# Kernel optimization log

Measured on AMD Instinct MI355X. Metric: run time of the kernel, lower is better.

Reference implementation:

```python
import jax, jax.numpy as jnp
import numpy as np

BITS = 8
BOUND = 2 ** (BITS - 1) - 1  # 127, symmetric int8 as in AQT IntNumerics


def setup_inputs() -> dict:
    key = jax.random.key(0)
    k1, k2 = jax.random.split(key)
    lhs = jax.random.normal(k1, (8192, 4096), dtype=jnp.float32)
    rhs = jax.random.normal(k2, (4096, 4096), dtype=jnp.float32)
    return {"lhs": lhs, "rhs": rhs}


def reference(lhs, rhs):
    # Per-channel symmetric scales over the contracting dim (AQT calibration:
    # abs-max / bound). lhs contracts axis 1, rhs contracts axis 0, per
    # dimension_numbers (((1,),(0,)),((),())).
    lhs_scale = jnp.max(jnp.abs(lhs), axis=1, keepdims=True) / BOUND  # [M,1]
    rhs_scale = jnp.max(jnp.abs(rhs), axis=0, keepdims=True) / BOUND  # [1,N]
    lhs_scale = jnp.where(lhs_scale == 0, jnp.ones_like(lhs_scale), lhs_scale)
    rhs_scale = jnp.where(rhs_scale == 0, jnp.ones_like(rhs_scale), rhs_scale)

    # Quantize: round-to-nearest, clip to [-127, 127], store as int8.
    qlhs = jnp.clip(jnp.round(lhs / lhs_scale), -BOUND, BOUND).astype(jnp.int8)
    qrhs = jnp.clip(jnp.round(rhs / rhs_scale), -BOUND, BOUND).astype(jnp.int8)

    # Integer matmul with int32 accumulation (the AQT quantized dot_general).
    acc = jax.lax.dot_general(
        qlhs, qrhs,
        dimension_numbers=(((1,), (0,)), ((), ())),
        preferred_element_type=jnp.int32,
    )  # [M, N] int32

    # Inline dequant by transposed scales (scale_t): [M,1] * [1,N].
    return acc.astype(jnp.float32) * lhs_scale * rhs_scale
```

## Files before the change

### kernel.cpp

```cpp
#include <hip/hip_runtime.h>
#include <stdint.h>

#define M_DIM 8192
#define N_DIM 4096
#define K_DIM 4096

typedef int v4i __attribute__((ext_vector_type(4)));

typedef __attribute__((address_space(1))) const void gas_void;
typedef __attribute__((address_space(3))) void las_void;

__device__ __forceinline__ void async_copy16(const uint8_t* g, uint8_t* l) {
    __builtin_amdgcn_global_load_lds((gas_void*)g, (las_void*)l, 16, 0, 0);
}

__device__ __forceinline__ int quant1(float x, float scale) {
    float q = __builtin_rintf(x / scale);
    q = fminf(127.0f, fmaxf(-127.0f, q));
    return (int)q;
}

__device__ __forceinline__ uint32_t pack4(int q0, int q1, int q2, int q3) {
    return (uint32_t)(q0 & 255) | ((uint32_t)(q1 & 255) << 8) |
           ((uint32_t)(q2 & 255) << 16) | ((uint32_t)(q3 & 255) << 24);
}

__global__ __launch_bounds__(256) void quant_lhs_kernel(
    const float* __restrict__ lhs, uint8_t* __restrict__ qlhs,
    float* __restrict__ lhs_scale) {
    const int row = blockIdx.x;
    const int tid = threadIdx.x;
    const float4* src = (const float4*)(lhs + (size_t)row * K_DIM);

    float4 v[4];
    float m = 0.0f;
#pragma unroll
    for (int i = 0; i < 4; ++i) {
        v[i] = src[tid + i * 256];
        m = fmaxf(m, fmaxf(fmaxf(fabsf(v[i].x), fabsf(v[i].y)),
                           fmaxf(fabsf(v[i].z), fabsf(v[i].w))));
    }
#pragma unroll
    for (int off = 32; off > 0; off >>= 1)
        m = fmaxf(m, __shfl_down(m, off, 64));

    __shared__ float wmax[4];
    if ((tid & 63) == 0) wmax[tid >> 6] = m;
    __syncthreads();
    const float mm = fmaxf(fmaxf(wmax[0], wmax[1]), fmaxf(wmax[2], wmax[3]));
    const float scale = (mm == 0.0f) ? 1.0f : mm / 127.0f;
    if (tid == 0) lhs_scale[row] = scale;

    uint32_t* dst = (uint32_t*)(qlhs + (size_t)row * K_DIM);
#pragma unroll
    for (int i = 0; i < 4; ++i) {
        dst[tid + i * 256] = pack4(quant1(v[i].x, scale), quant1(v[i].y, scale),
                                   quant1(v[i].z, scale), quant1(v[i].w, scale));
    }
}

__global__ __launch_bounds__(256) void rhs_max_kernel(
    const float* __restrict__ rhs, uint32_t* __restrict__ maxbits) {
    const int c4 = (blockIdx.x * 256 + threadIdx.x) * 4;
    const int r0 = blockIdx.y * 32;
    float m0 = 0.0f, m1 = 0.0f, m2 = 0.0f, m3 = 0.0f;
#pragma unroll
    for (int r = 0; r < 32; ++r) {
        const float4 v = *(const float4*)(rhs + (size_t)(r0 + r) * N_DIM + c4);
        m0 = fmaxf(m0, fabsf(v.x));
        m1 = fmaxf(m1, fabsf(v.y));
        m2 = fmaxf(m2, fabsf(v.z));
        m3 = fmaxf(m3, fabsf(v.w));
    }
    atomicMax(&maxbits[c4 + 0], __float_as_uint(m0));
    atomicMax(&maxbits[c4 + 1], __float_as_uint(m1));
    atomicMax(&maxbits[c4 + 2], __float_as_uint(m2));
    atomicMax(&maxbits[c4 + 3], __float_as_uint(m3));
}

__global__ __launch_bounds__(256) void quant_rhs_t_kernel(
    const float* __restrict__ rhs, const uint32_t* __restrict__ maxbits,
    uint8_t* __restrict__ qrhsT) {
    __shared__ __align__(16) uint8_t tile[64 * 132];
    const int nbase = blockIdx.x * 64;
    const int kbase = blockIdx.y * 128;
    const int tid = threadIdx.x;

    const int n0 = (tid & 15) * 4;
    float s[4];
#pragma unroll
    for (int j = 0; j < 4; ++j) {
        const float m = __uint_as_float(maxbits[nbase + n0 + j]);
        s[j] = (m == 0.0f) ? 1.0f : m / 127.0f;
    }

#pragma unroll
    for (int p = 0; p < 2; ++p) {
        const int k0 = (tid >> 4) * 4 + p * 64;
        int q[4][4];
#pragma unroll
        for (int i = 0; i < 4; ++i) {
            const float4 v = *(const float4*)(
                rhs + (size_t)(kbase + k0 + i) * N_DIM + nbase + n0);
            q[i][0] = quant1(v.x, s[0]);
            q[i][1] = quant1(v.y, s[1]);
            q[i][2] = quant1(v.z, s[2]);
            q[i][3] = quant1(v.w, s[3]);
        }
#pragma unroll
        for (int j = 0; j < 4; ++j) {
            *(uint32_t*)(tile + (n0 + j) * 132 + k0) =
                pack4(q[0][j], q[1][j], q[2][j], q[3][j]);
        }
    }
    __syncthreads();

#pragma unroll
    for (int p = 0; p < 2; ++p) {
        const int c = tid + p * 256;
        const int n = c >> 3;
        const int g = c & 7;
        uint32_t d[4];
#pragma unroll
        for (int w = 0; w < 4; ++w)
            d[w] = *(const uint32_t*)(tile + n * 132 + g * 16 + w * 4);
        uint4 u;
        u.x = d[0]; u.y = d[1]; u.z = d[2]; u.w = d[3];
        *(uint4*)(qrhsT + (size_t)(nbase + n) * K_DIM + kbase + g * 16) = u;
    }
}

__global__ __launch_bounds__(512, 2) void gemm_i8_kernel(
    const uint8_t* __restrict__ qlhs, const uint8_t* __restrict__ qrhsT,
    const float* __restrict__ lhs_scale, const uint32_t* __restrict__ maxbits,
    float* __restrict__ out) {
    extern __shared__ __align__(16) uint8_t smem[];

    const int tid = threadIdx.x;
    const int wave = tid >> 6;
    const int lane = tid & 63;

    const int obid = blockIdx.y * 16 + blockIdx.x;
    const int xcd = obid & 7;
    const int local = obid >> 3;
    const int ty = (xcd >> 1) * 8 + (local >> 3);
    const int tx = (xcd & 1) * 8 + (local & 7);
    const int bm = ty * 256;
    const int bn = tx * 256;

    const int srow = tid >> 2;
    const int gsrc = (((tid & 3) ^ ((tid >> 3) & 3)) << 4);
    const uint8_t* gA = qlhs + (size_t)(bm + srow) * K_DIM + gsrc;
    const uint8_t* gA2 = gA + (size_t)128 * K_DIM;
    const uint8_t* gB = qrhsT + (size_t)(bn + srow) * K_DIM + gsrc;
    const uint8_t* gB2 = gB + (size_t)128 * K_DIM;
    const uint32_t stO = (uint32_t)tid * 16u;

    const int wm = (wave >> 2) * 128;
    const int wn = (wave & 3) * 64;
    const uint32_t fg = (uint32_t)((((lane >> 4) ^ ((lane >> 1) & 3)) << 4));
    const uint32_t aoff = (uint32_t)((wm + (lane & 15)) * 64) + fg;
    const uint32_t boff = 16384u + (uint32_t)((wn + (lane & 15)) * 64) + fg;

    v4i acc[8][4] = {};

    v4i Xb0, Xb1, Xb2, Xb3, Xa0, Xa1;
    v4i Yb0, Yb1, Yb2, Yb3, Ya0, Ya1;

#define FENCE() asm volatile("" ::: "memory")
#define LGKM(n)                                                 \
    do {                                                        \
        asm volatile("s_waitcnt lgkmcnt(" #n ")" ::: "memory"); \
        __builtin_amdgcn_sched_barrier(0);                      \
    } while (0)
#define MFMA4(C, mi, av)                                                       \
    do {                                                                       \
        acc[mi][0] = __builtin_amdgcn_mfma_i32_16x16x64_i8(av, C##b0,          \
                                                           acc[mi][0], 0, 0, 0); \
        acc[mi][1] = __builtin_amdgcn_mfma_i32_16x16x64_i8(av, C##b1,          \
                                                           acc[mi][1], 0, 0, 0); \
        acc[mi][2] = __builtin_amdgcn_mfma_i32_16x16x64_i8(av, C##b2,          \
                                                           acc[mi][2], 0, 0, 0); \
        acc[mi][3] = __builtin_amdgcn_mfma_i32_16x16x64_i8(av, C##b3,          \
                                                           acc[mi][3], 0, 0, 0); \
    } while (0)

#define TILE(u, C, N)                                                   \
    do {                                                                \
        const uint8_t* const Cb = smem + ((u) << 15);                   \
        const uint8_t* const Nb = smem + ((((u) + 1) & 3) << 15);       \
        uint8_t* const Sb = smem + ((((u) + 3) & 3) << 15);             \
               \
        async_copy16(gA, Sb + stO);                                     \
        async_copy16(gA2, Sb + 8192 + stO);                             \
        async_copy16(gB, Sb + 16384 + stO);                             \
        async_copy16(gB2, Sb + 24576 + stO);                            \
        if (tt + (u) < 60) {                                            \
            gA += 64; gA2 += 64; gB += 64; gB2 += 64;                   \
        }                                                               \
        FENCE();                                                        \
        v4i va2, va3, va4, va5, va6, va7;                               \
        va2 = *(const v4i*)(Cb + aoff + 2048);                          \
        va3 = *(const v4i*)(Cb + aoff + 3072);                          \
        FENCE();                                                        \
        __builtin_amdgcn_s_setprio(1);                                  \
        MFMA4(C, 0, C##a0);                                             \
        va4 = *(const v4i*)(Cb + aoff + 4096);                          \
        va5 = *(const v4i*)(Cb + aoff + 5120);                          \
        FENCE();                                                        \
        MFMA4(C, 1, C##a1);                                             \
        va6 = *(const v4i*)(Cb + aoff + 6144);                          \
        va7 = *(const v4i*)(Cb + aoff + 7168);                          \
        FENCE();                                                        \
        LGKM(5);                                                        \
        MFMA4(C, 2, va2);                                               \
        N##b0 = *(const v4i*)(Nb + boff + 0);                           \
        N##b1 = *(const v4i*)(Nb + boff + 1024);                        \
        N##b2 = *(const v4i*)(Nb + boff + 2048);                        \
        N##b3 = *(const v4i*)(Nb + boff + 3072);                        \
        FENCE();                                                        \
        LGKM(8);                                                        \
        MFMA4(C, 3, va3);                                               \
        N##a0 = *(const v4i*)(Nb + aoff + 0);                           \
        N##a1 = *(const v4i*)(Nb + aoff + 1024);                        \
        FENCE();                                                        \
        LGKM(9);                                                        \
        MFMA4(C, 4, va4);                                               \
        LGKM(8);                                                        \
        MFMA4(C, 5, va5);                                               \
        LGKM(7);                                                        \
        MFMA4(C, 6, va6);                                               \
        LGKM(6);                                                        \
        MFMA4(C, 7, va7);                                               \
        __builtin_amdgcn_s_setprio(0);                                  \
        asm volatile("s_waitcnt vmcnt(4)" ::: "memory");                \
        __builtin_amdgcn_s_barrier();                                   \
        asm volatile("s_waitcnt lgkmcnt(0)" ::: "memory");              \
        __builtin_amdgcn_sched_barrier(0);                              \
    } while (0)

#pragma unroll
    for (int p = 0; p < 3; ++p) {
        uint8_t* sb = smem + (p << 15);
        async_copy16(gA, sb + stO);
        async_copy16(gA2, sb + 8192 + stO);
        async_copy16(gB, sb + 16384 + stO);
        async_copy16(gB2, sb + 24576 + stO);
        gA += 64; gA2 += 64; gB += 64; gB2 += 64;
    }
    asm volatile("s_waitcnt vmcnt(4)" ::: "memory");
    __builtin_amdgcn_s_barrier();

    Xb0 = *(const v4i*)(smem + boff + 0);
    Xb1 = *(const v4i*)(smem + boff + 1024);
    Xb2 = *(const v4i*)(smem + boff + 2048);
    Xb3 = *(const v4i*)(smem + boff + 3072);
    Xa0 = *(const v4i*)(smem + aoff + 0);
    Xa1 = *(const v4i*)(smem + aoff + 1024);
    asm volatile("s_waitcnt lgkmcnt(0)" ::: "memory");
    __builtin_amdgcn_sched_barrier(0);

#pragma unroll 1
    for (int tt = 0; tt < 64; tt += 4) {
        TILE(0, X, Y);
        TILE(1, Y, X);
        TILE(2, X, Y);
        TILE(3, Y, X);
    }
    asm volatile("s_waitcnt vmcnt(0)" ::: "memory");

    const int r0 = bm + wm + (lane >> 4) * 4;
    const int c0 = bn + wn + (lane & 15);
    float rsv[4];
#pragma unroll
    for (int ni = 0; ni < 4; ++ni) {
        const float m = __uint_as_float(maxbits[c0 + ni * 16]);
        rsv[ni] = (m == 0.0f) ? 1.0f : m / 127.0f;
    }
#pragma unroll
    for (int mi = 0; mi < 8; ++mi) {
        float ls[4];
#pragma unroll
        for (int r = 0; r < 4; ++r) ls[r] = lhs_scale[r0 + mi * 16 + r];
#pragma unroll
        for (int ni = 0; ni < 4; ++ni) {
            float* o = out + (size_t)(r0 + mi * 16) * N_DIM + c0 + ni * 16;
#pragma unroll
            for (int r = 0; r < 4; ++r)
                o[(size_t)r * N_DIM] = (float)acc[mi][ni][r] * ls[r] * rsv[ni];
        }
    }
#undef FENCE
#undef LGKM
#undef MFMA4
#undef TILE
}

extern "C" void kernel_launch(void* const* d_in, const int* in_sizes, int n_in,
                              void* d_out, int out_size, void* d_ws,
                              size_t ws_size, hipStream_t stream) {
    const float* lhs = (const float*)d_in[0];
    const float* rhs = (const float*)d_in[1];
    float* out = (float*)d_out;

    uint8_t* ws = (uint8_t*)d_ws;
    uint8_t* qlhs = ws;
    uint8_t* qrhsT = ws + 33554432u;
    float* lhs_scale = (float*)(ws + 50331648u);
    uint32_t* maxbits = (uint32_t*)(ws + 50380800u);

    static bool attr_set = false;
    if (!attr_set) {
        hipFuncSetAttribute((const void*)gemm_i8_kernel,
                            hipFuncAttributeMaxDynamicSharedMemorySize,
                            131072);
        attr_set = true;
    }

    hipMemsetAsync(maxbits, 0, N_DIM * sizeof(uint32_t), stream);

    quant_lhs_kernel<<<M_DIM, 256, 0, stream>>>(lhs, qlhs, lhs_scale);
    rhs_max_kernel<<<dim3(N_DIM / 1024, 128), 256, 0, stream>>>(rhs, maxbits);
    quant_rhs_t_kernel<<<dim3(N_DIM / 64, K_DIM / 128), 256, 0, stream>>>(
        rhs, maxbits, qrhsT);
    gemm_i8_kernel<<<dim3(N_DIM / 256, M_DIM / 256), 512, 131072, stream>>>(
        qlhs, qrhsT, lhs_scale, maxbits, out);
}
```

Baseline: 405.7 us.

## Shrink GEMM block tile to 256x128 with 3-stage LDS pipeline for higher occupancy

The int8 GEMM block tile shrinks from 256x256 to 256x128, so the grid grows to 32x32 and the XCD-aware remap changes to match. Each wave now computes 64x64 with a 4x4 accumulator, and the 4-deep LDS ring with register double-buffering becomes a 3-stage ring of 24KB stages. The simpler per-tile schedule issues all fragment loads first, then waits on lgkm counts between MFMA groups. The aim is to fit more blocks per CU (launch bounds 4, 72KB LDS) and hide latency through occupancy, at the cost of lower arithmetic intensity per block and more global and LDS traffic per MFMA.

```diff
diff --git a/kernel.cpp b/kernel.cpp
--- a/kernel.cpp
+++ b/kernel.cpp
@@ -130,7 +130,7 @@
     }
 }
 
-__global__ __launch_bounds__(512, 2) void gemm_i8_kernel(
+__global__ __launch_bounds__(512, 4) void gemm_i8_kernel(
     const uint8_t* __restrict__ qlhs, const uint8_t* __restrict__ qrhsT,
     const float* __restrict__ lhs_scale, const uint32_t* __restrict__ maxbits,
     float* __restrict__ out) {
@@ -140,32 +140,28 @@
     const int wave = tid >> 6;
     const int lane = tid & 63;
 
-    const int obid = blockIdx.y * 16 + blockIdx.x;
+    const int obid = blockIdx.y * 32 + blockIdx.x;
     const int xcd = obid & 7;
     const int local = obid >> 3;
-    const int ty = (xcd >> 1) * 8 + (local >> 3);
-    const int tx = (xcd & 1) * 8 + (local & 7);
+    const int ty = (xcd >> 2) * 16 + (local >> 3);
+    const int tx = (xcd & 3) * 8 + (local & 7);
     const int bm = ty * 256;
-    const int bn = tx * 256;
+    const int bn = tx * 128;
 
     const int srow = tid >> 2;
     const int gsrc = (((tid & 3) ^ ((tid >> 3) & 3)) << 4);
     const uint8_t* gA = qlhs + (size_t)(bm + srow) * K_DIM + gsrc;
     const uint8_t* gA2 = gA + (size_t)128 * K_DIM;
     const uint8_t* gB = qrhsT + (size_t)(bn + srow) * K_DIM + gsrc;
-    const uint8_t* gB2 = gB + (size_t)128 * K_DIM;
     const uint32_t stO = (uint32_t)tid * 16u;
 
-    const int wm = (wave >> 2) * 128;
-    const int wn = (wave & 3) * 64;
+    const int wm = (wave >> 1) * 64;
+    const int wn = (wave & 1) * 64;
     const uint32_t fg = (uint32_t)((((lane >> 4) ^ ((lane >> 1) & 3)) << 4));
     const uint32_t aoff = (uint32_t)((wm + (lane & 15)) * 64) + fg;
     const uint32_t boff = 16384u + (uint32_t)((wn + (lane & 15)) * 64) + fg;
 
-    v4i acc[8][4] = {};
-
-    v4i Xb0, Xb1, Xb2, Xb3, Xa0, Xa1;
-    v4i Yb0, Yb1, Yb2, Yb3, Ya0, Ya1;
+    v4i acc[4][4] = {};
 
 #define FENCE() asm volatile("" ::: "memory")
 #define LGKM(n)                                                 \
@@ -173,100 +169,79 @@
         asm volatile("s_waitcnt lgkmcnt(" #n ")" ::: "memory"); \
         __builtin_amdgcn_sched_barrier(0);                      \
     } while (0)
-#define MFMA4(C, mi, av)                                                       \
+#define MFMA4(mi, av)                                                          \
     do {                                                                       \
-        acc[mi][0] = __builtin_amdgcn_mfma_i32_16x16x64_i8(av, C##b0,          \
+        acc[mi][0] = __builtin_amdgcn_mfma_i32_16x16x64_i8(av, vb0,            \
                                                            acc[mi][0], 0, 0, 0); \
-        acc[mi][1] = __builtin_amdgcn_mfma_i32_16x16x64_i8(av, C##b1,          \
+        acc[mi][1] = __builtin_amdgcn_mfma_i32_16x16x64_i8(av, vb1,            \
                                                            acc[mi][1], 0, 0, 0); \
-        acc[mi][2] = __builtin_amdgcn_mfma_i32_16x16x64_i8(av, C##b2,          \
+        acc[mi][2] = __builtin_amdgcn_mfma_i32_16x16x64_i8(av, vb2,            \
                                                            acc[mi][2], 0, 0, 0); \
-        acc[mi][3] = __builtin_amdgcn_mfma_i32_16x16x64_i8(av, C##b3,          \
+        acc[mi][3] = __builtin_amdgcn_mfma_i32_16x16x64_i8(av, vb3,            \
                                                            acc[mi][3], 0, 0, 0); \
     } while (0)
 
-#define TILE(u, C, N)                                                   \
+#define TILE(Cs, Ss, t, DO_STAGE)                                       \
     do {                                                                \
-        const uint8_t* const Cb = smem + ((u) << 15);                   \
-        const uint8_t* const Nb = smem + ((((u) + 1) & 3) << 15);       \
-        uint8_t* const Sb = smem + ((((u) + 3) & 3) << 15);             \
+        v4i vb0, vb1, vb2, vb3, va0, va1, va2, va3;                     \
                \
-        async_copy16(gA, Sb + stO);                                     \
-        async_copy16(gA2, Sb + 8192 + stO);                             \
-        async_copy16(gB, Sb + 16384 + stO);                             \
-        async_copy16(gB2, Sb + 24576 + stO);                            \
-        if (tt + (u) < 60) {                                            \
-            gA += 64; gA2 += 64; gB += 64; gB2 += 64;                   \
+        vb0 = *(const v4i*)((Cs) + boff + 0);                           \
+        vb1 = *(const v4i*)((Cs) + boff + 1024);                        \
+        vb2 = *(const v4i*)((Cs) + boff + 2048);                        \
+        vb3 = *(const v4i*)((Cs) + boff + 3072);                        \
+        FENCE();                                                        \
+        va0 = *(const v4i*)((Cs) + aoff + 0);                           \
+        FENCE();                                                        \
+        va1 = *(const v4i*)((Cs) + aoff + 1024);                        \
+        FENCE();                                                        \
+        va2 = *(const v4i*)((Cs) + aoff + 2048);                        \
+        FENCE();                                                        \
+        va3 = *(const v4i*)((Cs) + aoff + 3072);                        \
+        FENCE();                                                        \
+        if (DO_STAGE) {                                                 \
+            async_copy16(gA, (Ss) + stO);                               \
+            async_copy16(gA2, (Ss) + 8192 + stO);                       \
+            async_copy16(gB, (Ss) + 16384 + stO);                       \
+            if ((t) < 62) {                                             \
+                gA += 64; gA2 += 64; gB += 64;                          \
+            }                                                           \
         }                                                               \
         FENCE();                                                        \
-        v4i va2, va3, va4, va5, va6, va7;                               \
-        va2 = *(const v4i*)(Cb + aoff + 2048);                          \
-        va3 = *(const v4i*)(Cb + aoff + 3072);                          \
-        FENCE();                                                        \
         __builtin_amdgcn_s_setprio(1);                                  \
-        MFMA4(C, 0, C##a0);                                             \
-        va4 = *(const v4i*)(Cb + aoff + 4096);                          \
-        va5 = *(const v4i*)(Cb + aoff + 5120);                          \
-        FENCE();                                                        \
-        MFMA4(C, 1, C##a1);                                             \
-        va6 = *(const v4i*)(Cb + aoff + 6144);                          \
-        va7 = *(const v4i*)(Cb + aoff + 7168);                          \
-        FENCE();                                                        \
-        LGKM(5);                                                        \
-        MFMA4(C, 2, va2);                                               \
-        N##b0 = *(const v4i*)(Nb + boff + 0);                           \
-        N##b1 = *(const v4i*)(Nb + boff + 1024);                        \
-        N##b2 = *(const v4i*)(Nb + boff + 2048);                        \
-        N##b3 = *(const v4i*)(Nb + boff + 3072);                        \
-        FENCE();                                                        \
-        LGKM(8);                                                        \
-        MFMA4(C, 3, va3);                                               \
-        N##a0 = *(const v4i*)(Nb + aoff + 0);                           \
-        N##a1 = *(const v4i*)(Nb + aoff + 1024);                        \
-        FENCE();                                                        \
-        LGKM(9);                                                        \
-        MFMA4(C, 4, va4);                                               \
-        LGKM(8);                                                        \
-        MFMA4(C, 5, va5);                                               \
-        LGKM(7);                                                        \
-        MFMA4(C, 6, va6);                                               \
-        LGKM(6);                                                        \
-        MFMA4(C, 7, va7);                                               \
+        LGKM(3); MFMA4(0, va0);                                         \
+        LGKM(2); MFMA4(1, va1);                                         \
+        LGKM(1); MFMA4(2, va2);                                         \
+        LGKM(0); MFMA4(3, va3);                                         \
         __builtin_amdgcn_s_setprio(0);                                  \
-        asm volatile("s_waitcnt vmcnt(4)" ::: "memory");                \
-        __builtin_amdgcn_s_barrier();                                   \
-        asm volatile("s_waitcnt lgkmcnt(0)" ::: "memory");              \
-        __builtin_amdgcn_sched_barrier(0);                              \
+        if (DO_STAGE) {                                                 \
+            asm volatile("s_waitcnt vmcnt(3)" ::: "memory");            \
+            __builtin_amdgcn_s_barrier();                               \
+        }                                                               \
     } while (0)
 
-#pragma unroll
-    for (int p = 0; p < 3; ++p) {
-        uint8_t* sb = smem + (p << 15);
-        async_copy16(gA, sb + stO);
-        async_copy16(gA2, sb + 8192 + stO);
-        async_copy16(gB, sb + 16384 + stO);
-        async_copy16(gB2, sb + 24576 + stO);
-        gA += 64; gA2 += 64; gB += 64; gB2 += 64;
-    }
-    asm volatile("s_waitcnt vmcnt(4)" ::: "memory");
+    uint8_t* const s0 = smem;
+    uint8_t* const s1 = smem + 24576;
+    uint8_t* const s2 = smem + 49152;
+
+    async_copy16(gA, s0 + stO);
+    async_copy16(gA2, s0 + 8192 + stO);
+    async_copy16(gB, s0 + 16384 + stO);
+    gA += 64; gA2 += 64; gB += 64;
+    async_copy16(gA, s1 + stO);
+    async_copy16(gA2, s1 + 8192 + stO);
+    async_copy16(gB, s1 + 16384 + stO);
+    gA += 64; gA2 += 64; gB += 64;
+    asm volatile("s_waitcnt vmcnt(3)" ::: "memory");
     __builtin_amdgcn_s_barrier();
 
-    Xb0 = *(const v4i*)(smem + boff + 0);
-    Xb1 = *(const v4i*)(smem + boff + 1024);
-    Xb2 = *(const v4i*)(smem + boff + 2048);
-    Xb3 = *(const v4i*)(smem + boff + 3072);
-    Xa0 = *(const v4i*)(smem + aoff + 0);
-    Xa1 = *(const v4i*)(smem + aoff + 1024);
-    asm volatile("s_waitcnt lgkmcnt(0)" ::: "memory");
-    __builtin_amdgcn_sched_barrier(0);
-
 #pragma unroll 1
-    for (int tt = 0; tt < 64; tt += 4) {
-        TILE(0, X, Y);
-        TILE(1, Y, X);
-        TILE(2, X, Y);
-        TILE(3, Y, X);
-    }
+    for (int tt = 0; tt < 63; tt += 3) {
+        TILE(s0, s2, tt + 0, 1);
+        TILE(s1, s0, tt + 1, 1);
+        TILE(s2, s1, tt + 2, 1);
+    }
+    TILE(s0, s1, 63, 0);
+
     asm volatile("s_waitcnt vmcnt(0)" ::: "memory");
 
     const int r0 = bm + wm + (lane >> 4) * 4;
@@ -278,7 +253,7 @@
         rsv[ni] = (m == 0.0f) ? 1.0f : m / 127.0f;
     }
 #pragma unroll
-    for (int mi = 0; mi < 8; ++mi) {
+    for (int mi = 0; mi < 4; ++mi) {
         float ls[4];
 #pragma unroll
         for (int r = 0; r < 4; ++r) ls[r] = lhs_scale[r0 + mi * 16 + r];
@@ -313,7 +288,7 @@
     if (!attr_set) {
         hipFuncSetAttribute((const void*)gemm_i8_kernel,
                             hipFuncAttributeMaxDynamicSharedMemorySize,
-                            131072);
+                            73728);
         attr_set = true;
     }
 
@@ -323,6 +298,6 @@
     rhs_max_kernel<<<dim3(N_DIM / 1024, 128), 256, 0, stream>>>(rhs, maxbits);
     quant_rhs_t_kernel<<<dim3(N_DIM / 64, K_DIM / 128), 256, 0, stream>>>(
         rhs, maxbits, qrhsT);
-    gemm_i8_kernel<<<dim3(N_DIM / 256, M_DIM / 256), 512, 131072, stream>>>(
+    gemm_i8_kernel<<<dim3(32, 32), 512, 73728, stream>>>(
         qlhs, qrhsT, lhs_scale, maxbits, out);
 }
```

Result: slower. 415.8 us (+2.5%).
